# Performance work log

Hardware: AMD Instinct MI355X
Metric: run time of the kernel (lower is better)

## Reference

```python
import jax, jax.numpy as jnp
import numpy as np

NUM_HEADS = 48
EMBED_DIM = 768


def setup_inputs() -> dict:
    key = jax.random.key(0)
    ks = jax.random.split(key, 12)
    b, n, e, n_exp = 2, 512, EMBED_DIM, 256
    m = n + n_exp  # expanded kv length (periodic images appended)
    s = 0.02
    return {
        "query": jax.random.normal(ks[0], (b, n, e), jnp.float32),
        "attn_bias": jax.random.normal(ks[1], (b * NUM_HEADS, n, m), jnp.float32),
        "delta_pos": jax.random.normal(ks[2], (b, n, m, 3), jnp.float32),
        "outcell_index": jax.random.randint(ks[3], (b, n_exp), 0, n, jnp.int32),
        "Wq": jax.random.normal(ks[4], (e, e), jnp.float32) * s,
        "bq": jnp.zeros((e,), jnp.float32),
        "Wk": jax.random.normal(ks[5], (e, e), jnp.float32) * s,
        "bk": jnp.zeros((e,), jnp.float32),
        "Wv": jax.random.normal(ks[6], (e, e), jnp.float32) * s,
        "bv": jnp.zeros((e,), jnp.float32),
        "w_force": jax.random.normal(ks[7], (e,), jnp.float32) * s,
    }


def reference(query, attn_bias, delta_pos, outcell_index, Wq, bq, Wk, bk, Wv, bv, w_force):
    b, n, e = query.shape
    H = NUM_HEADS
    d = e // H
    scaling = d ** (-0.5)

    def proj(W, bias):
        # [b, n, e] -> [b, H, n, d]
        return (query @ W.T + bias).reshape(b, n, H, d).transpose(0, 2, 1, 3)

    q = proj(Wq, bq) * scaling
    k = proj(Wk, bk)
    v = proj(Wv, bv)

    # periodic-image KV expansion: gather nodes along axis 2, concat
    idx = outcell_index[:, None, :, None]  # [b, 1, n_exp, 1] broadcasts over H, d
    k = jnp.concatenate([k, jnp.take_along_axis(k, idx, axis=2)], axis=2)
    v = jnp.concatenate([v, jnp.take_along_axis(v, idx, axis=2)], axis=2)
    m = k.shape[2]  # n_node_expand

    attn = jnp.einsum('bhnd,bhmd->bhnm', q, k)
    probs = jax.nn.softmax(attn + attn_bias.reshape(b, H, n, m), axis=-1)
    # dropout p=0.1 is identity in eval mode

    # position-weighted value aggregation: [b,h,n,m]*[b,n,m,3] contracted with v over m
    x = jnp.einsum('bhnm,bnmc,bhmd->bnchd', probs, delta_pos, v).reshape(b, n, 3, e)
    force = jnp.einsum('bnce,e->bnc', x, w_force).astype(jnp.float32)  # [b, n, 3]
    return force
```

## Files before the change

### kernel.cpp

```cpp
#include <hip/hip_runtime.h>
#include <cstdint>
#include <cstddef>

#define BDIM 2
#define NQ 512
#define NEXP 256
#define MDIM 768
#define HN 48
#define DD 16
#define ED 768

typedef short v8s __attribute__((ext_vector_type(8)));
typedef float v4f __attribute__((ext_vector_type(4)));

__global__ void prep_kernel(const float* __restrict__ Wv, const float* __restrict__ bv,
                            const float* __restrict__ wf,
                            float* __restrict__ wve, float* __restrict__ ube) {
  int h = blockIdx.x;
  float wl[DD];
#pragma unroll
  for (int d = 0; d < DD; ++d) wl[d] = wf[h * DD + d];
  for (int k = threadIdx.x; k < ED; k += blockDim.x) {
    float s = 0.f;
#pragma unroll
    for (int d = 0; d < DD; ++d) s = fmaf(wl[d], Wv[(size_t)(h * DD + d) * ED + k], s);
    wve[(size_t)h * ED + k] = s;
  }
  if (threadIdx.x == 0) {
    float s = 0.f;
#pragma unroll
    for (int d = 0; d < DD; ++d) s = fmaf(wl[d], bv[h * DD + d], s);
    ube[h] = s;
  }
}

__global__ __launch_bounds__(256) void convert_kernel(
    const float* __restrict__ query, const float* __restrict__ Wq,
    const float* __restrict__ Wk, const float* __restrict__ wve,
    ushort* __restrict__ Abf, ushort* __restrict__ Bbf) {
  const int id = blockIdx.x * 256 + threadIdx.x;
  const float* src = nullptr;
  ushort* dst;
  if (id < 98304) {
    const int off = id * 8;
    src = query + off;
    dst = Abf + off;
  } else {
    const int id2 = id - 98304;
    const int r = id2 / 96;
    const int k = (id2 - r * 96) * 8;
    dst = Bbf + (size_t)r * 768 + k;
    if (r < 768)       src = Wq + (size_t)r * 768 + k;
    else if (r < 1536) src = Wk + (size_t)(r - 768) * 768 + k;
    else if (r < 1584) src = wve + (size_t)(r - 1536) * 768 + k;
  }
  union { ushort s[8]; uint4 v; } p;
  if (src) {
    const float4 v0 = *(const float4*)src;
    const float4 v1 = *(const float4*)(src + 4);
    const float vv[8] = {v0.x, v0.y, v0.z, v0.w, v1.x, v1.y, v1.z, v1.w};
#pragma unroll
    for (int i = 0; i < 8; ++i) {
      union { float f; uint32_t u; } c; c.f = vv[i];
      p.s[i] = (ushort)((c.u + 0x7FFFu + ((c.u >> 16) & 1u)) >> 16);
    }
  } else {
#pragma unroll
    for (int i = 0; i < 8; ++i) p.s[i] = 0;
  }
  *(uint4*)dst = p.v;
}

__global__ __launch_bounds__(256) void proj_mfma(
    const ushort* __restrict__ Abf, const ushort* __restrict__ Bbf,
    const float* __restrict__ bq, const float* __restrict__ bk,
    const float* __restrict__ ube,
    float* __restrict__ qs, float* __restrict__ ke, float* __restrict__ ub) {
  __shared__ __align__(16) ushort As[4][4][16][8];
  __shared__ __align__(16) ushort Bs[4][64][8];
  const int tid = threadIdx.x;
  const int wave = tid >> 6, lane = tid & 63;
  const int m0 = blockIdx.y * 64, n0 = blockIdx.x * 64;
  const int arow = tid >> 2;
  const int aseg = tid & 3;
  v4f acc[4] = {v4f{0,0,0,0}, v4f{0,0,0,0}, v4f{0,0,0,0}, v4f{0,0,0,0}};

  for (int k0 = 0; k0 < ED; k0 += 32) {
    __syncthreads();
    *(uint4*)&As[arow >> 4][aseg][arow & 15][0] =
        *(const uint4*)&Abf[(size_t)(m0 + arow) * ED + k0 + aseg * 8];
    *(uint4*)&Bs[aseg][arow][0] =
        *(const uint4*)&Bbf[(size_t)(n0 + arow) * ED + k0 + aseg * 8];
    __syncthreads();
    const v8s af = *(const v8s*)&As[wave][lane >> 4][lane & 15][0];
#pragma unroll
    for (int nt = 0; nt < 4; ++nt) {
      const v8s bfr = *(const v8s*)&Bs[lane >> 4][nt * 16 + (lane & 15)][0];
      acc[nt] = __builtin_amdgcn_mfma_f32_16x16x32_bf16(af, bfr, acc[nt], 0, 0, 0);
    }
  }

#pragma unroll
  for (int nt = 0; nt < 4; ++nt) {
    const int c = n0 + nt * 16 + (lane & 15);
    if (c >= 1584) continue;
#pragma unroll
    for (int r = 0; r < 4; ++r) {
      const int row = m0 + wave * 16 + (lane >> 4) * 4 + r;
      const int b = row >> 9, n = row & 511;
      const float val = acc[nt][r];
      if (c < 768) {
        qs[(size_t)(b * NQ + n) * ED + c] = (val + bq[c]) * 0.25f;
      } else if (c < 1536) {
        const int ck = c - 768;
        const int hh = ck >> 4, dd = ck & 15;
        ke[(size_t)((b * HN + hh) * DD + dd) * MDIM + n] = val + bk[ck];
      } else {
        const int hh = c - 1536;
        ub[(size_t)(b * HN + hh) * MDIM + n] = val + ube[hh];
      }
    }
  }
}

__global__ void gather_kernel(const int* __restrict__ idx, float* __restrict__ ke,
                              float* __restrict__ ub) {
  const int id = blockIdx.x * 256 + threadIdx.x;
  const int N1 = BDIM * HN * DD * NEXP;
  if (id < N1) {
    int j = id & (NEXP - 1);
    int d = (id >> 8) & (DD - 1);
    int hb = id >> 12;
    int n = idx[(hb / HN) * NEXP + j];
    float* row = ke + (size_t)(hb * DD + d) * MDIM;
    row[NQ + j] = row[n];
  } else {
    int id2 = id - N1;
    if (id2 < BDIM * HN * NEXP) {
      int j = id2 & (NEXP - 1);
      int hb = id2 >> 8;
      int n = idx[(hb / HN) * NEXP + j];
      float* row = ub + (size_t)hb * MDIM;
      row[NQ + j] = row[n];
    }
  }
}

__device__ __forceinline__ void fma4(float4& a, float q, const float4& k) {
  a.x = fmaf(q, k.x, a.x); a.y = fmaf(q, k.y, a.y);
  a.z = fmaf(q, k.z, a.z); a.w = fmaf(q, k.w, a.w);
}

__device__ __forceinline__ void gload_lds16(const float4* g, float4* l) {
  __builtin_amdgcn_global_load_lds(
      (const __attribute__((address_space(1))) void*)g,
      (__attribute__((address_space(3))) void*)l, 16, 0, 0);
}

__global__ __launch_bounds__(192) void fused_kernel(
    const float* __restrict__ qs, const float* __restrict__ ke, const float* __restrict__ ub,
    const float* __restrict__ bias, float* __restrict__ Wp) {
  __shared__ __align__(16) float Ks[8 * MDIM];
  __shared__ float red[2][3][4];
  const int bid = blockIdx.x;
  const int b = bid & 1;
  const int hg = (bid >> 1) & 3;
  const int n0 = (bid >> 3) * 4;
  const int g = threadIdx.x >> 6;
  const int lane = threadIdx.x & 63;
  const int hbase = hg * 12;

  float4 a[4];
  float4 wacc[4] = {};

#pragma unroll
  for (int i = 0; i < 4; ++i)
    a[i] = ((const float4*)(bias + (size_t)((b * HN + hbase) * NQ + n0 + i) * MDIM))[g * 64 + lane];

  for (int hi = 0; hi < 12; ++hi) {
    const int h = hbase + hi;
    const size_t krow0 = (size_t)(b * HN + h) * DD;
    const float4* kl = (const float4*)Ks;

#pragma unroll
    for (int dh = 0; dh < 2; ++dh) {
      float4 qh[4];
#pragma unroll
      for (int i = 0; i < 4; ++i)
        qh[i] = ((const float4*)(qs + (size_t)(b * NQ + n0 + i) * ED + h * DD))[dh * 2];
      float4 qh2[4];
#pragma unroll
      for (int i = 0; i < 4; ++i)
        qh2[i] = ((const float4*)(qs + (size_t)(b * NQ + n0 + i) * ED + h * DD))[dh * 2 + 1];

#pragma unroll
      for (int j = 0; j < 8; ++j) {
        const float4* src = (const float4*)(ke + (krow0 + dh * 8 + j) * MDIM) + g * 64 + lane;
        gload_lds16(src, (float4*)Ks + j * 192 + g * 64);
      }
      asm volatile("s_waitcnt vmcnt(0)" ::: "memory");

#pragma unroll
      for (int d4 = 0; d4 < 2; ++d4) {
#pragma unroll
        for (int dd = 0; dd < 4; ++dd) {
          const float4 k0 = kl[(d4 * 4 + dd) * 192 + g * 64 + lane];
#pragma unroll
          for (int i = 0; i < 4; ++i) {
            const float4 qv = d4 ? qh2[i] : qh[i];
            const float qd = (dd == 0) ? qv.x : (dd == 1) ? qv.y : (dd == 2) ? qv.z : qv.w;
            fma4(a[i], qd, k0);
          }
        }
      }
    }

    float mx[4];
#pragma unroll
    for (int i = 0; i < 4; ++i) {
      float m = fmaxf(fmaxf(a[i].x, a[i].y), fmaxf(a[i].z, a[i].w));
#pragma unroll
      for (int sh = 32; sh > 0; sh >>= 1) m = fmaxf(m, __shfl_xor(m, sh));
      mx[i] = m;
    }
    if (lane == 0) {
#pragma unroll
      for (int i = 0; i < 4; ++i) red[0][g][i] = mx[i];
    }
    __syncthreads();
#pragma unroll
    for (int i = 0; i < 4; ++i)
      mx[i] = fmaxf(red[0][0][i], fmaxf(red[0][1][i], red[0][2][i]));

    float l[4];
#pragma unroll
    for (int i = 0; i < 4; ++i) {
      a[i].x = __expf(a[i].x - mx[i]);
      a[i].y = __expf(a[i].y - mx[i]);
      a[i].z = __expf(a[i].z - mx[i]);
      a[i].w = __expf(a[i].w - mx[i]);
      float s = a[i].x + a[i].y + a[i].z + a[i].w;
#pragma unroll
      for (int sh = 32; sh > 0; sh >>= 1) s += __shfl_xor(s, sh);
      l[i] = s;
    }
    if (lane == 0) {
#pragma unroll
      for (int i = 0; i < 4; ++i) red[1][g][i] = l[i];
    }
    __syncthreads();

    const float4 uu = ((const float4*)(ub + (size_t)(b * HN + h) * MDIM))[g * 64 + lane];
#pragma unroll
    for (int i = 0; i < 4; ++i) {
      const float inv = 1.0f / (red[1][0][i] + red[1][1][i] + red[1][2][i]);
      wacc[i].x = fmaf(a[i].x * inv, uu.x, wacc[i].x);
      wacc[i].y = fmaf(a[i].y * inv, uu.y, wacc[i].y);
      wacc[i].z = fmaf(a[i].z * inv, uu.z, wacc[i].z);
      wacc[i].w = fmaf(a[i].w * inv, uu.w, wacc[i].w);
    }

    if (hi < 11) {
#pragma unroll
      for (int i = 0; i < 4; ++i)
        a[i] = ((const float4*)(bias + (size_t)((b * HN + h + 1) * NQ + n0 + i) * MDIM))[g * 64 + lane];
    }
  }

  float4* wp = (float4*)Wp;
#pragma unroll
  for (int i = 0; i < 4; ++i)
    wp[((size_t)(b * NQ + n0 + i) * 4 + hg) * 192 + g * 64 + lane] = wacc[i];
}

__global__ __launch_bounds__(256) void force_kernel(
    const float* __restrict__ Wp, const float* __restrict__ dp, float* __restrict__ out) {
  const int wave = threadIdx.x >> 6;
  const int lane = threadIdx.x & 63;
  const int row = blockIdx.x * 4 + wave;
  const float4* wp = (const float4*)Wp;
  float4 ws[3];
#pragma unroll
  for (int j = 0; j < 3; ++j) {
    float4 s = wp[((size_t)row * 4 + 0) * 192 + lane + 64 * j];
#pragma unroll
    for (int hg = 1; hg < 4; ++hg) {
      const float4 t = wp[((size_t)row * 4 + hg) * 192 + lane + 64 * j];
      s.x += t.x; s.y += t.y; s.z += t.z; s.w += t.w;
    }
    ws[j] = s;
  }
  const float* dpp = dp + (size_t)row * MDIM * 3;
  float f0 = 0.f, f1 = 0.f, f2 = 0.f;
#pragma unroll
  for (int j = 0; j < 3; ++j) {
    const float4 w = ws[j];
    const int m0 = j * 256 + lane * 4;
    const float4* dv = (const float4*)(dpp + (size_t)m0 * 3);
    const float4 d0 = dv[0], d1 = dv[1], d2 = dv[2];
    f0 = fmaf(w.x, d0.x, f0); f0 = fmaf(w.y, d0.w, f0); f0 = fmaf(w.z, d1.z, f0); f0 = fmaf(w.w, d2.y, f0);
    f1 = fmaf(w.x, d0.y, f1); f1 = fmaf(w.y, d1.x, f1); f1 = fmaf(w.z, d1.w, f1); f1 = fmaf(w.w, d2.z, f1);
    f2 = fmaf(w.x, d0.z, f2); f2 = fmaf(w.y, d1.y, f2); f2 = fmaf(w.z, d2.x, f2); f2 = fmaf(w.w, d2.w, f2);
  }
#pragma unroll
  for (int sh = 32; sh > 0; sh >>= 1) {
    f0 += __shfl_xor(f0, sh);
    f1 += __shfl_xor(f1, sh);
    f2 += __shfl_xor(f2, sh);
  }
  if (lane == 0) {
    float* op = out + (size_t)row * 3;
    op[0] = f0; op[1] = f1; op[2] = f2;
  }
}

extern "C" void kernel_launch(void* const* d_in, const int* in_sizes, int n_in,
                              void* d_out, int out_size, void* d_ws, size_t ws_size,
                              hipStream_t stream) {
  const float* query     = (const float*)d_in[0];
  const float* attn_bias = (const float*)d_in[1];
  const float* delta_pos = (const float*)d_in[2];
  const int*   outcell   = (const int*)d_in[3];
  const float* Wq = (const float*)d_in[4];
  const float* bq = (const float*)d_in[5];
  const float* Wk = (const float*)d_in[6];
  const float* bk = (const float*)d_in[7];
  const float* Wv = (const float*)d_in[8];
  const float* bv = (const float*)d_in[9];
  const float* wf = (const float*)d_in[10];
  float* out = (float*)d_out;
  float* ws  = (float*)d_ws;

  float* wve  = ws;
  float* ube  = ws + 36864;
  float* qsb  = ws + 36928;
  float* keb  = ws + 823360;
  float* ubb  = ws + 2003008;
  float* Wpb  = ws + 2076736;
  ushort* Abf = (ushort*)(ws + 5222464);
  ushort* Bbf = (ushort*)(ws + 5615680);

  prep_kernel<<<HN, 256, 0, stream>>>(Wv, bv, wf, wve, ube);
  convert_kernel<<<984, 256, 0, stream>>>(query, Wq, Wk, wve, Abf, Bbf);
  proj_mfma<<<dim3(25, 16), 256, 0, stream>>>(Abf, Bbf, bq, bk, ube, qsb, keb, ubb);
  gather_kernel<<<1632, 256, 0, stream>>>(outcell, keb, ubb);
  fused_kernel<<<1024, 192, 0, stream>>>(qsb, keb, ubb, attn_bias, Wpb);
  force_kernel<<<256, 256, 0, stream>>>(Wpb, delta_pos, out);
}
```

Baseline: 298.8 us.

## Restructure fused attention kernel to 8 rows per block with direct K loads

The fused attention/softmax kernel now handles 8 query rows per block with 384 threads, each thread owning 2 columns, instead of 4 rows with 192 threads owning 4 columns. The LDS staging of K via global_load_lds and its waitcnt is dropped in favour of direct float2 global loads, so each K load is reused across 8 rows. The next head's bias prefetch is issued earlier, right after the scores are formed. The aim is more K reuse per load, fewer blocks and no LDS round trip, at the cost of smaller per-thread vector loads and a 6-wave reduction per row.

```diff
diff --git a/kernel.cpp b/kernel.cpp
--- a/kernel.cpp
+++ b/kernel.cpp
@@ -146,131 +146,112 @@
   }
 }
 
-__device__ __forceinline__ void fma4(float4& a, float q, const float4& k) {
-  a.x = fmaf(q, k.x, a.x); a.y = fmaf(q, k.y, a.y);
-  a.z = fmaf(q, k.z, a.z); a.w = fmaf(q, k.w, a.w);
-}
-
-__device__ __forceinline__ void gload_lds16(const float4* g, float4* l) {
-  __builtin_amdgcn_global_load_lds(
-      (const __attribute__((address_space(1))) void*)g,
-      (__attribute__((address_space(3))) void*)l, 16, 0, 0);
-}
-
-__global__ __launch_bounds__(192) void fused_kernel(
+__global__ __launch_bounds__(384) void fused_kernel(
     const float* __restrict__ qs, const float* __restrict__ ke, const float* __restrict__ ub,
     const float* __restrict__ bias, float* __restrict__ Wp) {
-  __shared__ __align__(16) float Ks[8 * MDIM];
-  __shared__ float red[2][3][4];
+  __shared__ float red[2][6][8];
   const int bid = blockIdx.x;
   const int b = bid & 1;
   const int hg = (bid >> 1) & 3;
-  const int n0 = (bid >> 3) * 4;
+  const int r0 = (bid >> 3) * 8;
   const int g = threadIdx.x >> 6;
   const int lane = threadIdx.x & 63;
   const int hbase = hg * 12;
-
-  float4 a[4];
-  float4 wacc[4] = {};
-
-#pragma unroll
-  for (int i = 0; i < 4; ++i)
-    a[i] = ((const float4*)(bias + (size_t)((b * HN + hbase) * NQ + n0 + i) * MDIM))[g * 64 + lane];
-
+  const int col = g * 128 + lane * 2;
+
+  float2 a[8];
+  float2 wacc[8];
+#pragma unroll
+  for (int i = 0; i < 8; ++i) wacc[i] = float2{0.f, 0.f};
+
+#pragma unroll
+  for (int i = 0; i < 8; ++i)
+    a[i] = *(const float2*)(bias + (size_t)((b * HN + hbase) * NQ + r0 + i) * MDIM + col);
+
+#pragma unroll 1
   for (int hi = 0; hi < 12; ++hi) {
     const int h = hbase + hi;
-    const size_t krow0 = (size_t)(b * HN + h) * DD;
-    const float4* kl = (const float4*)Ks;
-
-#pragma unroll
-    for (int dh = 0; dh < 2; ++dh) {
-      float4 qh[4];
-#pragma unroll
-      for (int i = 0; i < 4; ++i)
-        qh[i] = ((const float4*)(qs + (size_t)(b * NQ + n0 + i) * ED + h * DD))[dh * 2];
-      float4 qh2[4];
-#pragma unroll
-      for (int i = 0; i < 4; ++i)
-        qh2[i] = ((const float4*)(qs + (size_t)(b * NQ + n0 + i) * ED + h * DD))[dh * 2 + 1];
-
-#pragma unroll
-      for (int j = 0; j < 8; ++j) {
-        const float4* src = (const float4*)(ke + (krow0 + dh * 8 + j) * MDIM) + g * 64 + lane;
-        gload_lds16(src, (float4*)Ks + j * 192 + g * 64);
+    const float* kb = ke + (size_t)(b * HN + h) * DD * MDIM + col;
+
+    float2 s[8];
+#pragma unroll
+    for (int i = 0; i < 8; ++i) s[i] = float2{0.f, 0.f};
+#pragma unroll
+    for (int c = 0; c < 4; ++c) {
+      const float2 k0 = *(const float2*)(kb + (c * 4 + 0) * MDIM);
+      const float2 k1 = *(const float2*)(kb + (c * 4 + 1) * MDIM);
+      const float2 k2 = *(const float2*)(kb + (c * 4 + 2) * MDIM);
+      const float2 k3 = *(const float2*)(kb + (c * 4 + 3) * MDIM);
+#pragma unroll
+      for (int i = 0; i < 8; ++i) {
+        const float4 q4 = *(const float4*)(qs + (size_t)(b * NQ + r0 + i) * ED + h * DD + c * 4);
+        s[i].x = fmaf(q4.x, k0.x, s[i].x); s[i].y = fmaf(q4.x, k0.y, s[i].y);
+        s[i].x = fmaf(q4.y, k1.x, s[i].x); s[i].y = fmaf(q4.y, k1.y, s[i].y);
+        s[i].x = fmaf(q4.z, k2.x, s[i].x); s[i].y = fmaf(q4.z, k2.y, s[i].y);
+        s[i].x = fmaf(q4.w, k3.x, s[i].x); s[i].y = fmaf(q4.w, k3.y, s[i].y);
       }
-      asm volatile("s_waitcnt vmcnt(0)" ::: "memory");
-
-#pragma unroll
-      for (int d4 = 0; d4 < 2; ++d4) {
-#pragma unroll
-        for (int dd = 0; dd < 4; ++dd) {
-          const float4 k0 = kl[(d4 * 4 + dd) * 192 + g * 64 + lane];
-#pragma unroll
-          for (int i = 0; i < 4; ++i) {
-            const float4 qv = d4 ? qh2[i] : qh[i];
-            const float qd = (dd == 0) ? qv.x : (dd == 1) ? qv.y : (dd == 2) ? qv.z : qv.w;
-            fma4(a[i], qd, k0);
-          }
-        }
-      }
-    }
-
-    float mx[4];
-#pragma unroll
-    for (int i = 0; i < 4; ++i) {
-      float m = fmaxf(fmaxf(a[i].x, a[i].y), fmaxf(a[i].z, a[i].w));
+    }
+
+#pragma unroll
+    for (int i = 0; i < 8; ++i) { s[i].x += a[i].x; s[i].y += a[i].y; }
+    if (hi < 11) {
+#pragma unroll
+      for (int i = 0; i < 8; ++i)
+        a[i] = *(const float2*)(bias + (size_t)((b * HN + h + 1) * NQ + r0 + i) * MDIM + col);
+    }
+
+    float mx[8];
+#pragma unroll
+    for (int i = 0; i < 8; ++i) {
+      float m = fmaxf(s[i].x, s[i].y);
 #pragma unroll
       for (int sh = 32; sh > 0; sh >>= 1) m = fmaxf(m, __shfl_xor(m, sh));
       mx[i] = m;
     }
     if (lane == 0) {
 #pragma unroll
-      for (int i = 0; i < 4; ++i) red[0][g][i] = mx[i];
+      for (int i = 0; i < 8; ++i) red[0][g][i] = mx[i];
     }
     __syncthreads();
 #pragma unroll
-    for (int i = 0; i < 4; ++i)
-      mx[i] = fmaxf(red[0][0][i], fmaxf(red[0][1][i], red[0][2][i]));
-
-    float l[4];
-#pragma unroll
-    for (int i = 0; i < 4; ++i) {
-      a[i].x = __expf(a[i].x - mx[i]);
-      a[i].y = __expf(a[i].y - mx[i]);
-      a[i].z = __expf(a[i].z - mx[i]);
-      a[i].w = __expf(a[i].w - mx[i]);
-      float s = a[i].x + a[i].y + a[i].z + a[i].w;
-#pragma unroll
-      for (int sh = 32; sh > 0; sh >>= 1) s += __shfl_xor(s, sh);
-      l[i] = s;
+    for (int i = 0; i < 8; ++i) {
+      float m = red[0][0][i];
+#pragma unroll
+      for (int gg = 1; gg < 6; ++gg) m = fmaxf(m, red[0][gg][i]);
+      mx[i] = m;
+    }
+
+    float l[8];
+#pragma unroll
+    for (int i = 0; i < 8; ++i) {
+      s[i].x = __expf(s[i].x - mx[i]);
+      s[i].y = __expf(s[i].y - mx[i]);
+      float t = s[i].x + s[i].y;
+#pragma unroll
+      for (int sh = 32; sh > 0; sh >>= 1) t += __shfl_xor(t, sh);
+      l[i] = t;
     }
     if (lane == 0) {
 #pragma unroll
-      for (int i = 0; i < 4; ++i) red[1][g][i] = l[i];
+      for (int i = 0; i < 8; ++i) red[1][g][i] = l[i];
     }
     __syncthreads();
 
-    const float4 uu = ((const float4*)(ub + (size_t)(b * HN + h) * MDIM))[g * 64 + lane];
-#pragma unroll
-    for (int i = 0; i < 4; ++i) {
-      const float inv = 1.0f / (red[1][0][i] + red[1][1][i] + red[1][2][i]);
-      wacc[i].x = fmaf(a[i].x * inv, uu.x, wacc[i].x);
-      wacc[i].y = fmaf(a[i].y * inv, uu.y, wacc[i].y);
-      wacc[i].z = fmaf(a[i].z * inv, uu.z, wacc[i].z);
-      wacc[i].w = fmaf(a[i].w * inv, uu.w, wacc[i].w);
-    }
-
-    if (hi < 11) {
-#pragma unroll
-      for (int i = 0; i < 4; ++i)
-        a[i] = ((const float4*)(bias + (size_t)((b * HN + h + 1) * NQ + n0 + i) * MDIM))[g * 64 + lane];
-    }
-  }
-
-  float4* wp = (float4*)Wp;
-#pragma unroll
-  for (int i = 0; i < 4; ++i)
-    wp[((size_t)(b * NQ + n0 + i) * 4 + hg) * 192 + g * 64 + lane] = wacc[i];
+    const float2 u2 = *(const float2*)(ub + (size_t)(b * HN + h) * MDIM + col);
+#pragma unroll
+    for (int i = 0; i < 8; ++i) {
+      float lg = red[1][0][i];
+#pragma unroll
+      for (int gg = 1; gg < 6; ++gg) lg += red[1][gg][i];
+      const float inv = 1.0f / lg;
+      wacc[i].x = fmaf(s[i].x * inv, u2.x, wacc[i].x);
+      wacc[i].y = fmaf(s[i].y * inv, u2.y, wacc[i].y);
+    }
+  }
+
+#pragma unroll
+  for (int i = 0; i < 8; ++i)
+    *(float2*)(Wp + ((size_t)(b * NQ + r0 + i) * 4 + hg) * MDIM + col) = wacc[i];
 }
 
 __global__ __launch_bounds__(256) void force_kernel(
@@ -344,6 +325,6 @@
   convert_kernel<<<984, 256, 0, stream>>>(query, Wq, Wk, wve, Abf, Bbf);
   proj_mfma<<<dim3(25, 16), 256, 0, stream>>>(Abf, Bbf, bq, bk, ube, qsb, keb, ubb);
   gather_kernel<<<1632, 256, 0, stream>>>(outcell, keb, ubb);
-  fused_kernel<<<1024, 192, 0, stream>>>(qsb, keb, ubb, attn_bias, Wpb);
+  fused_kernel<<<512, 384, 0, stream>>>(qsb, keb, ubb, attn_bias, Wpb);
   force_kernel<<<256, 256, 0, stream>>>(Wpb, delta_pos, out);
 }
```

New measurement: 317.0 us. 1.06x slower.
